# Kernel optimization log

Hardware: AMD Instinct MI355X
Metric: run time of the kernel (lower is better)

## Reference

```python
import jax, jax.numpy as jnp
import numpy as np

D_IN = 1024
D_OUT = 1024


def setup_inputs() -> dict:
    key = jax.random.key(0)
    ks = jax.random.split(key, 7)
    B, S = 4, 2048
    x = jax.random.normal(ks[0], (B, S, D_IN), dtype=jnp.float32)
    s = 1.0 / np.sqrt(D_IN)
    Wq = jax.random.uniform(ks[1], (D_IN, D_OUT), jnp.float32, -s, s)
    Wk = jax.random.uniform(ks[2], (D_IN, D_OUT), jnp.float32, -s, s)
    Wv = jax.random.uniform(ks[3], (D_IN, D_OUT), jnp.float32, -s, s)
    bq = jax.random.uniform(ks[4], (D_OUT,), jnp.float32, -s, s)
    bk = jax.random.uniform(ks[5], (D_OUT,), jnp.float32, -s, s)
    bv = jax.random.uniform(ks[6], (D_OUT,), jnp.float32, -s, s)
    return {"x": x, "Wq": Wq, "Wk": Wk, "Wv": Wv, "bq": bq, "bk": bk, "bv": bv}


def reference(x, Wq, Wk, Wv, bq, bk, bv):
    # x: [B, S, d_in]
    B, S, _ = x.shape
    q = x @ Wq + bq            # [B, S, d_out]
    k = x @ Wk + bk
    v = x @ Wv + bv
    scale = 1.0 / jnp.sqrt(jnp.asarray(q.shape[-1], q.dtype))
    scores = jnp.einsum('bqd,bkd->bqk', q, k)  # [B, S, S]
    causal = jnp.tril(jnp.ones((S, S), dtype=bool))
    scores = jnp.where(causal, scores, -jnp.inf)
    attn = jax.nn.softmax(scores * scale, axis=-1)
    return jnp.einsum('bqk,bkd->bqd', attn, v)
```

## Files before the change

### kernel.cpp

```cpp
#include <hip/hip_runtime.h>
#include <cstdint>

#define DEV __device__ __forceinline__

typedef __attribute__((ext_vector_type(4))) float f32x4;
typedef __attribute__((ext_vector_type(8))) short short8;
typedef __attribute__((ext_vector_type(4))) unsigned short u16x4;

constexpr int BS  = 4;
constexpr int SEQ = 2048;

DEV ushort f2b(float f){
  uint32_t u = __builtin_bit_cast(uint32_t, f);
  u += 0x7fffu + ((u >> 16) & 1u);
  return (ushort)(u >> 16);
}
DEV float b2f(ushort h){
  uint32_t u = (uint32_t)h << 16;
  return __builtin_bit_cast(float, u);
}

DEV void gload_lds16(const void* g, void* l){
  __builtin_amdgcn_global_load_lds(
      (const __attribute__((address_space(1))) unsigned int*)g,
      (__attribute__((address_space(3))) unsigned int*)l, 16, 0, 0);
}

#define BAR()    __builtin_amdgcn_s_barrier()
#define PRIO(x)  __builtin_amdgcn_s_setprio(x)
#define SCHEDB() __builtin_amdgcn_sched_barrier(0)
#define LGKM0()  asm volatile("s_waitcnt lgkmcnt(0)" ::: "memory")
#define WAITV(n) asm volatile("s_waitcnt vmcnt(" #n ")" ::: "memory")

__global__ __launch_bounds__(256) void convert_f2b8(const float* __restrict__ src,
                                                    ushort* __restrict__ dst){
  long i = (long)blockIdx.x * 256 + threadIdx.x;
  const f32x4* s4 = (const f32x4*)src;
  f32x4 a = s4[i*2], b = s4[i*2+1];
  short8 o;
  o[0]=(short)f2b(a[0]); o[1]=(short)f2b(a[1]); o[2]=(short)f2b(a[2]); o[3]=(short)f2b(a[3]);
  o[4]=(short)f2b(b[0]); o[5]=(short)f2b(b[1]); o[6]=(short)f2b(b[2]); o[7]=(short)f2b(b[3]);
  ((short8*)dst)[i] = o;
}

__global__ __launch_bounds__(256) void transpose_f2b(const float* __restrict__ src,
                                                     ushort* __restrict__ dst,
                                                     int R, int C){
  __shared__ float t[32][33];
  int c0 = blockIdx.x * 32, r0 = blockIdx.y * 32;
  int tx = threadIdx.x, ty = threadIdx.y;
  #pragma unroll
  for (int k=0;k<4;k++) t[ty+k*8][tx] = src[(long)(r0+ty+k*8)*C + c0+tx];
  __syncthreads();
  #pragma unroll
  for (int k=0;k<4;k++) dst[(long)(c0+ty+k*8)*R + r0+tx] = f2b(t[tx][ty+k*8]);
}

__global__ __launch_bounds__(256) void transpose_b2b(const ushort* __restrict__ src,
                                                     ushort* __restrict__ dst,
                                                     int R, int C){
  __shared__ ushort t[32][33];
  int c0 = blockIdx.x * 32, r0 = blockIdx.y * 32;
  int tx = threadIdx.x, ty = threadIdx.y;
  #pragma unroll
  for (int k=0;k<4;k++) t[ty+k*8][tx] = src[(long)(r0+ty+k*8)*C + c0+tx];
  __syncthreads();
  #pragma unroll
  for (int k=0;k<4;k++) dst[(long)(c0+ty+k*8)*R + r0+tx] = t[tx][ty+k*8];
}

struct GArgs {
  const ushort* A;  long lda; long aBS;
  const ushort* Bm; long ldb; long bBS;
  void* C;          long ldc; long cBS;
  const float* b0; const float* b1; const float* b2;
  int K;
};

__global__ __launch_bounds__(512, 2) void gemmA_qkv(GArgs g){
  extern __shared__ char sm[];
  const int tid = threadIdx.x;
  const int wid = tid >> 6, lane = tid & 63;
  const int wr = wid >> 2, wc = wid & 3;
  const int lr = lane & 15, lk = lane >> 4;
  const int f5 = ((lr >> 3) & 1) << 5;

  const int fid = blockIdx.x;
  const int xcd = fid & 7, j = fid >> 3;
  const int m0 = (xcd * 4 + (j & 3)) * 256;
  const int n0 = (j >> 2) * 192;

  const long lda2 = g.lda * 2, ldb2 = g.ldb * 2;
  const int skk = tid >> 8;
  const int srr = (tid >> 2) & 63;
  const int scc = tid & 3;
  const int scb = (scc * 16) ^ (((srr >> 3) & 1) << 5);
  const char* aU0 = (const char*)g.A  + (long)(m0       + srr)*lda2 + skk*64 + scb;
  const char* aU1 = (const char*)g.A  + (long)(m0 +  64 + srr)*lda2 + skk*64 + scb;
  const char* aU2 = (const char*)g.A  + (long)(m0 + 128 + srr)*lda2 + skk*64 + scb;
  const char* aU3 = (const char*)g.A  + (long)(m0 + 192 + srr)*lda2 + skk*64 + scb;
  const char* bU0 = (const char*)g.Bm + (long)(n0       + srr)*ldb2 + skk*64 + scb;
  const char* bU1 = (const char*)g.Bm + (long)(n0 +  64 + srr)*ldb2 + skk*64 + scb;
  const char* bU2 = (const char*)g.Bm + (long)(n0 + 128 + srr)*ldb2 + skk*64 + scb;
  const int dst = tid * 16;

#define STA(u, cb, k0) gload_lds16(aU##u + (k0)*2, sm + (cb)*57344 + u*8192 + dst)
#define STB(u, cb, k0) gload_lds16(bU##u + (k0)*2, sm + (cb)*57344 + 32768 + u*8192 + dst)

  int aoff[8], boff[3];
  #pragma unroll
  for (int mm=0;mm<8;mm++)
    aoff[mm] = wr*16384 + (mm>>2)*8192 + (mm&3)*1024 + lr*64 + ((lk*16) ^ f5);
  #pragma unroll
  for (int nn=0;nn<3;nn++){
    int br = wc*48 + nn*16 + lr;
    boff[nn] = 32768 + (br>>6)*8192 + (br&63)*64 + ((lk*16) ^ f5);
  }

  f32x4 acc[8][3];
  #pragma unroll
  for (int m=0;m<8;m++)
    #pragma unroll
    for (int n=0;n<3;n++) acc[m][n] = f32x4{0.f,0.f,0.f,0.f};

  const int NT = g.K >> 6;
  STA(0,0,0); STA(1,0,0); STA(2,0,0); STA(3,0,0);
  STB(0,0,0); STB(1,0,0); STB(2,0,0);
  STB(0,1,64); STB(1,1,64); STB(2,1,64);
  WAITV(3); BAR();

  short8 bf[3][2], af[2][2];
#define READ_AF(MB) \
    af[0][0] = *(const short8*)(base + aoff[MB  ]);        \
    af[0][1] = *(const short8*)(base + aoff[MB  ] + 4096); \
    af[1][0] = *(const short8*)(base + aoff[MB+1]);        \
    af[1][1] = *(const short8*)(base + aoff[MB+1] + 4096);
#define MFMA6(MB) \
    PRIO(1); \
    _Pragma("unroll") \
    for (int kk=0;kk<2;kk++) \
      _Pragma("unroll") \
      for (int mm=0;mm<2;mm++) \
        _Pragma("unroll") \
        for (int nn=0;nn<3;nn++) \
          acc[MB+mm][nn] = __builtin_amdgcn_mfma_f32_16x16x32_bf16(af[mm][kk], bf[nn][kk], acc[MB+mm][nn], 0,0,0); \
    PRIO(0);

  for (int t = 0; t < NT; ++t){
    const int c = t & 1;
    const char* base = sm + c*57344;
    const int kA = ((t+1) < NT ? (t+1) : NT-1) << 6;
    const int kB = ((t+2) < NT ? (t+2) : NT-1) << 6;
    STA(0, c^1, kA); STA(1, c^1, kA);
    #pragma unroll
    for (int nn=0;nn<3;nn++){
      bf[nn][0] = *(const short8*)(base + boff[nn]);
      bf[nn][1] = *(const short8*)(base + boff[nn] + 4096);
    }
    READ_AF(0);
    LGKM0(); SCHEDB();
    MFMA6(0);
    BAR();
    STA(2, c^1, kA); STA(3, c^1, kA);
    READ_AF(2);
    LGKM0(); SCHEDB();
    MFMA6(2);
    BAR();
    STB(0, c, kB); STB(1, c, kB);
    READ_AF(4);
    LGKM0(); SCHEDB();
    MFMA6(4);
    BAR();
    STB(2, c, kB);
    READ_AF(6);
    LGKM0(); SCHEDB();
    MFMA6(6);
    WAITV(3);
    BAR();
  }
  WAITV(0);
#undef STA
#undef STB
#undef READ_AF
#undef MFMA6

  #pragma unroll
  for (int nn=0;nn<3;nn++){
    int col  = n0 + wc*48 + nn*16 + lr;
    int sel  = col >> 10;
    int colq = col & 1023;
    const float* bp = (sel == 0) ? g.b0 : (sel == 1) ? g.b1 : g.b2;
    float bv = bp[colq];
    ushort* Cq = (ushort*)g.C + (long)sel * 8388608;
    #pragma unroll
    for (int mm=0;mm<8;mm++){
      int row0 = m0 + wr*128 + mm*16 + lk*4;
      #pragma unroll
      for (int i=0;i<4;i++)
        Cq[(long)(row0+i)*1024 + colq] = f2b(acc[mm][nn][i] + bv);
    }
  }
}

template<int MODE>
__global__ __launch_bounds__(512, 2) void gemmB(GArgs g){
  extern __shared__ char sm[];
  const int m0 = blockIdx.x * 128, n0 = blockIdx.y * 256;
  const int z  = blockIdx.z;
  if (MODE == 1 && n0 > m0 + 127) return;
  const int tid = threadIdx.x;
  const int wid = tid >> 6, lane = tid & 63;
  const int wr = wid >> 2, wc = wid & 3;
  const int lr = lane & 15, lk = lane >> 4;
  const int f5 = ((lr >> 3) & 1) << 5;

  const char* Ab = (const char*)(g.A  + (long)z * g.aBS);
  const char* Bb = (const char*)(g.Bm + (long)z * g.bBS);
  const long lda2 = g.lda * 2, ldb2 = g.ldb * 2;
  const int sr  = tid >> 2;
  const int scb = ((lane & 3) << 4) ^ (((sr >> 3) & 1) << 5);
  const char* ar0 = Ab + (long)(m0 + sr)*lda2 + scb;
  const char* br0 = Bb + (long)(n0 + sr      )*ldb2 + scb;
  const char* br1 = Bb + (long)(n0 + 128 + sr)*ldb2 + scb;
  const int dwo = wid << 10;

  auto ST = [&](const char* row, int c, int off, int k0){
    const char* p = row + k0*2;
    char* d = sm + c*49152 + off + dwo;
    gload_lds16(p,      d);
    gload_lds16(p + 64, d + 8192);
  };

  const int aoffs = (wr*64 + lr)*64 + ((lk*16) ^ f5);
  const int boffs = 16384 + (wc>>1)*16384 + ((wc&1)*64 + lr)*64 + ((lk*16) ^ f5);

  f32x4 acc[4][4];
  #pragma unroll
  for (int m=0;m<4;m++)
    #pragma unroll
    for (int n=0;n<4;n++) acc[m][n] = f32x4{0.f,0.f,0.f,0.f};

  const int Keff = (MODE == 2) ? (m0 + 128) : g.K;
  const int NT = Keff >> 6;
  ST(ar0, 0, 0, 0);
  ST(br0, 0, 16384, 0); ST(br1, 0, 32768, 0);
  ST(br0, 1, 16384, 64); ST(br1, 1, 32768, 64);
  WAITV(4); BAR();

  for (int t = 0; t < NT; ++t){
    const int c = t & 1;
    const char* base = sm + c*49152;
    const int kA = ((t+1) < NT ? (t+1) : NT-1) << 6;
    const int kB = ((t+2) < NT ? (t+2) : NT-1) << 6;
    short8 bf[4][2], af[2][2];
    ST(ar0, c^1, 0, kA);
    #pragma unroll
    for (int n=0;n<4;n++)
      #pragma unroll
      for (int kk=0;kk<2;kk++)
        bf[n][kk] = *(const short8*)(base + boffs + kk*8192 + n*1024);
    #pragma unroll
    for (int mm=0;mm<2;mm++)
      #pragma unroll
      for (int kk=0;kk<2;kk++)
        af[mm][kk] = *(const short8*)(base + aoffs + kk*8192 + mm*1024);
    LGKM0(); SCHEDB();
    PRIO(1);
    #pragma unroll
    for (int kk=0;kk<2;kk++)
      #pragma unroll
      for (int mm=0;mm<2;mm++)
        #pragma unroll
        for (int n=0;n<4;n++)
          acc[mm][n] = __builtin_amdgcn_mfma_f32_16x16x32_bf16(af[mm][kk], bf[n][kk], acc[mm][n], 0,0,0);
    PRIO(0);
    BAR();
    ST(br0, c, 16384, kB); ST(br1, c, 32768, kB);
    #pragma unroll
    for (int mm=0;mm<2;mm++)
      #pragma unroll
      for (int kk=0;kk<2;kk++)
        af[mm][kk] = *(const short8*)(base + aoffs + kk*8192 + (2+mm)*1024);
    LGKM0(); SCHEDB();
    PRIO(1);
    #pragma unroll
    for (int kk=0;kk<2;kk++)
      #pragma unroll
      for (int mm=0;mm<2;mm++)
        #pragma unroll
        for (int n=0;n<4;n++)
          acc[2+mm][n] = __builtin_amdgcn_mfma_f32_16x16x32_bf16(af[mm][kk], bf[n][kk], acc[2+mm][n], 0,0,0);
    PRIO(0);
    WAITV(4);
    BAR();
  }
  WAITV(0);

  long cz = (long)z * g.cBS;
  #pragma unroll
  for (int m=0;m<4;m++){
    int row0 = m0 + wr*64 + m*16 + lk*4;
    #pragma unroll
    for (int n=0;n<4;n++){
      int col = n0 + wc*64 + n*16 + lr;
      #pragma unroll
      for (int i=0;i<4;i++){
        long off = cz + (long)(row0+i)*g.ldc + col;
        if (MODE == 1) ((ushort*)g.C)[off] = f2b(acc[m][n][i]);
        else           ((float*)g.C)[off]  = acc[m][n][i];
      }
    }
  }
}

__global__ __launch_bounds__(256) void softmax_causal_b(const ushort* __restrict__ sc,
                                                        ushort* __restrict__ P){
  int row = blockIdx.x & (SEQ-1);
  int b   = blockIdx.x >> 11;
  const short8* srow = (const short8*)(sc + ((long)b*SEQ + row)*(long)SEQ);
  ushort* prow = P + ((long)b*SEQ + row)*(long)SEQ;
  int tid = threadIdx.x;
  int lane = tid & 63, wid = tid >> 6;
  const float scale = 0.03125f;
  float x[8]; float mx = -INFINITY;
  int base = tid * 8;
  if (base <= row){
    short8 v = srow[tid];
    #pragma unroll
    for (int j=0;j<8;j++){
      float t = (base + j <= row) ? b2f((ushort)v[j]) : -INFINITY;
      x[j] = t; mx = fmaxf(mx, t);
    }
  } else {
    #pragma unroll
    for (int j=0;j<8;j++) x[j] = -INFINITY;
  }
  #pragma unroll
  for (int off=1; off<64; off<<=1) mx = fmaxf(mx, __shfl_xor(mx, off));
  __shared__ float rb[8];
  if (lane == 0) rb[wid] = mx;
  __syncthreads();
  mx = fmaxf(fmaxf(rb[0],rb[1]), fmaxf(rb[2],rb[3]));
  float sum = 0.f; float e[8];
  #pragma unroll
  for (int i=0;i<8;i++){ e[i] = __expf((x[i]-mx)*scale); sum += e[i]; }
  #pragma unroll
  for (int off=1; off<64; off<<=1) sum += __shfl_xor(sum, off);
  if (lane == 0) rb[4+wid] = sum;
  __syncthreads();
  sum = (rb[4]+rb[5]) + (rb[6]+rb[7]);
  float inv = 1.0f / sum;
  int wlim = row | 127;
  if (base <= wlim){
    short8 o;
    #pragma unroll
    for (int j=0;j<8;j++) o[j] = (short)f2b(e[j]*inv);
    ((short8*)prow)[tid] = o;
  }
}

extern "C" void kernel_launch(void* const* d_in, const int* in_sizes, int n_in,
                              void* d_out, int out_size, void* d_ws, size_t ws_size,
                              hipStream_t stream){
  const float* x  = (const float*)d_in[0];
  const float* Wq = (const float*)d_in[1];
  const float* Wk = (const float*)d_in[2];
  const float* Wv = (const float*)d_in[3];
  const float* bq = (const float*)d_in[4];
  const float* bk = (const float*)d_in[5];
  const float* bv = (const float*)d_in[6];
  float* out = (float*)d_out;

  const long XB = 0;
  const long WT = 16777216;
  const long QB = 23068672;
  const long VT = 73400320;
  const long SC = 90177536;
  const long NEED = 157286400;
  const long PB = 0;
  if ((long)ws_size < NEED) return;

  char* ws = (char*)d_ws;
  ushort* xb = (ushort*)(ws + XB);
  ushort* wt = (ushort*)(ws + WT);
  ushort* qb = (ushort*)(ws + QB);
  ushort* kb = qb + 8388608;
  ushort* vb = qb + 16777216;
  ushort* vt = (ushort*)(ws + VT);
  ushort* sc = (ushort*)(ws + SC);
  ushort* pb = (ushort*)(ws + PB);

  hipFuncSetAttribute(reinterpret_cast<const void*>(&gemmA_qkv),
                      hipFuncAttributeMaxDynamicSharedMemorySize, 114688);
  hipFuncSetAttribute(reinterpret_cast<const void*>(&gemmB<1>),
                      hipFuncAttributeMaxDynamicSharedMemorySize, 98304);
  hipFuncSetAttribute(reinterpret_cast<const void*>(&gemmB<2>),
                      hipFuncAttributeMaxDynamicSharedMemorySize, 98304);

  dim3 tb(32, 8);

  convert_f2b8<<<4096, 256, 0, stream>>>(x, xb);
  transpose_f2b<<<dim3(32,32), tb, 0, stream>>>(Wq, wt + 0,       1024, 1024);
  transpose_f2b<<<dim3(32,32), tb, 0, stream>>>(Wk, wt + 1048576, 1024, 1024);
  transpose_f2b<<<dim3(32,32), tb, 0, stream>>>(Wv, wt + 2097152, 1024, 1024);

  GArgs pa{};
  pa.A = xb; pa.lda = 1024; pa.aBS = 0;
  pa.Bm = wt; pa.ldb = 1024; pa.bBS = 0;
  pa.C = (void*)qb; pa.ldc = 1024; pa.cBS = 0;
  pa.b0 = bq; pa.b1 = bk; pa.b2 = bv;
  pa.K = 1024;
  gemmA_qkv<<<512, 512, 114688, stream>>>(pa);

  transpose_b2b<<<dim3(32,256), tb, 0, stream>>>(vb, vt, 8192, 1024);

  GArgs sa{};
  sa.A = qb;  sa.lda = 1024; sa.aBS = (long)SEQ*1024;
  sa.Bm = kb; sa.ldb = 1024; sa.bBS = (long)SEQ*1024;
  sa.C = (void*)sc; sa.ldc = SEQ; sa.cBS = (long)SEQ*SEQ;
  sa.b0 = nullptr; sa.b1 = nullptr; sa.b2 = nullptr;
  sa.K = 1024;
  gemmB<1><<<dim3(16,8,4), 512, 98304, stream>>>(sa);

  softmax_causal_b<<<BS*SEQ, 256, 0, stream>>>(sc, pb);

  GArgs va{};
  va.A = pb;  va.lda = SEQ;  va.aBS = (long)SEQ*SEQ;
  va.Bm = vt; va.ldb = 8192; va.bBS = SEQ;
  va.C = (void*)out; va.ldc = 1024; va.cBS = (long)SEQ*1024;
  va.b0 = nullptr; va.b1 = nullptr; va.b2 = nullptr;
  va.K = SEQ;
  gemmB<2><<<dim3(16,4,4), 512, 98304, stream>>>(va);
}
```

Measured before the change: 173.8 us.

## Fuse exp into scores GEMM epilogue and defer softmax normalization to PV

```diff
diff --git a/kernel.cpp b/kernel.cpp
--- a/kernel.cpp
+++ b/kernel.cpp
@@ -30,6 +30,7 @@
 #define PRIO(x)  __builtin_amdgcn_s_setprio(x)
 #define SCHEDB() __builtin_amdgcn_sched_barrier(0)
 #define LGKM0()  asm volatile("s_waitcnt lgkmcnt(0)" ::: "memory")
+#define LGKM8()  asm volatile("s_waitcnt lgkmcnt(8)" ::: "memory")
 #define WAITV(n) asm volatile("s_waitcnt vmcnt(" #n ")" ::: "memory")
 
 __global__ __launch_bounds__(256) void convert_f2b8(const float* __restrict__ src,
@@ -43,17 +44,21 @@
   ((short8*)dst)[i] = o;
 }
 
-__global__ __launch_bounds__(256) void transpose_f2b(const float* __restrict__ src,
-                                                     ushort* __restrict__ dst,
-                                                     int R, int C){
+__global__ __launch_bounds__(256) void transpose_f2b3(const float* __restrict__ w0,
+                                                      const float* __restrict__ w1,
+                                                      const float* __restrict__ w2,
+                                                      ushort* __restrict__ dst){
   __shared__ float t[32][33];
+  const int zz = blockIdx.z;
+  const float* src = (zz == 0) ? w0 : (zz == 1) ? w1 : w2;
+  ushort* d = dst + (long)zz * 1048576;
   int c0 = blockIdx.x * 32, r0 = blockIdx.y * 32;
   int tx = threadIdx.x, ty = threadIdx.y;
   #pragma unroll
-  for (int k=0;k<4;k++) t[ty+k*8][tx] = src[(long)(r0+ty+k*8)*C + c0+tx];
+  for (int k=0;k<4;k++) t[ty+k*8][tx] = src[(long)(r0+ty+k*8)*1024 + c0+tx];
   __syncthreads();
   #pragma unroll
-  for (int k=0;k<4;k++) dst[(long)(c0+ty+k*8)*R + r0+tx] = f2b(t[tx][ty+k*8]);
+  for (int k=0;k<4;k++) d[(long)(c0+ty+k*8)*1024 + r0+tx] = f2b(t[tx][ty+k*8]);
 }
 
 __global__ __launch_bounds__(256) void transpose_b2b(const ushort* __restrict__ src,
@@ -202,12 +207,154 @@
   }
 }
 
-template<int MODE>
-__global__ __launch_bounds__(512, 2) void gemmB(GArgs g){
+__global__ __launch_bounds__(512, 2) void scores8p(GArgs g){
+  extern __shared__ char sm[];
+  const int m0 = blockIdx.x * 256, n0 = blockIdx.y * 256;
+  const int z  = blockIdx.z;
+  if (n0 > m0) return;
+  const int tid = threadIdx.x;
+  const int wid = tid >> 6, lane = tid & 63;
+  const int wr = wid >> 2, wc = wid & 3;
+  const int lr = lane & 15, lk = lane >> 4;
+
+  const char* Ab = (const char*)(g.A  + (long)z * g.aBS);
+  const char* Bb = (const char*)(g.Bm + (long)z * g.bBS);
+  const long lda2 = g.lda * 2, ldb2 = g.ldb * 2;
+  const int srow = tid >> 2;
+  const int scol = ((tid & 3) << 4) ^ (((tid >> 5) & 1) << 5);
+  const char* sA = Ab + (long)(m0 + srow) * lda2 + scol;
+  const char* sB = Bb + (long)(n0 + srow) * ldb2 + scol;
+  const int dst16 = tid << 4;
+
+  auto STAGE = [&](int tt, int which){
+    const char* s = (which < 2)
+        ? sA + (long)(which & 1) * 128 * lda2 + (long)tt * 128
+        : sB + (long)(which & 1) * 128 * ldb2 + (long)tt * 128;
+    char* d = sm + (tt & 1) * 65536 + which * 16384 + dst16;
+    gload_lds16(s,      d);
+    gload_lds16(s + 64, d + 8192);
+  };
+
+  int aoff[8], boff[4];
+  #pragma unroll
+  for (int mm = 0; mm < 8; mm++){
+    int r = mm * 16 + lr;
+    aoff[mm] = wr * 16384 + r * 64 + ((lk * 16) ^ (((r >> 3) & 1) << 5));
+  }
+  #pragma unroll
+  for (int nn = 0; nn < 4; nn++){
+    int rb = wc * 64 + nn * 16 + lr;
+    boff[nn] = 32768 + (rb >> 7) * 16384 + (rb & 127) * 64
+             + ((lk * 16) ^ (((rb >> 3) & 1) << 5));
+  }
+
+  f32x4 acc[8][4];
+  #pragma unroll
+  for (int m = 0; m < 8; m++)
+    #pragma unroll
+    for (int n = 0; n < 4; n++) acc[m][n] = f32x4{0.f,0.f,0.f,0.f};
+
+  const int NT = g.K >> 6;
+  STAGE(0,2); STAGE(0,3); STAGE(0,0); STAGE(0,1);
+  STAGE(1,2); STAGE(1,3);
+  WAITV(4); BAR();
+
+  short8 af[2][2], bf[4][2];
+#define READ_A(MB) \
+    af[0][0] = *(const short8*)(base + aoff[MB]);            \
+    af[0][1] = *(const short8*)(base + aoff[MB] + 8192);     \
+    af[1][0] = *(const short8*)(base + aoff[MB+1]);          \
+    af[1][1] = *(const short8*)(base + aoff[MB+1] + 8192);
+#define MFMA16(MB) \
+    PRIO(1); \
+    _Pragma("unroll") \
+    for (int kk = 0; kk < 2; kk++) \
+      _Pragma("unroll") \
+      for (int mm = 0; mm < 2; mm++) \
+        _Pragma("unroll") \
+        for (int nn = 0; nn < 4; nn++) \
+          acc[MB+mm][nn] = __builtin_amdgcn_mfma_f32_16x16x32_bf16(af[mm][kk], bf[nn][kk], acc[MB+mm][nn], 0,0,0); \
+    PRIO(0);
+
+  for (int t = 0; t < NT; ++t){
+    const char* base = sm + (t & 1) * 65536;
+    if (t + 1 < NT) STAGE(t+1, 0);
+    #pragma unroll
+    for (int nn = 0; nn < 4; nn++){
+      bf[nn][0] = *(const short8*)(base + boff[nn]);
+      bf[nn][1] = *(const short8*)(base + boff[nn] + 8192);
+    }
+    READ_A(0);
+    LGKM8();
+    SCHEDB(); BAR(); LGKM0(); SCHEDB();
+    MFMA16(0);
+    SCHEDB(); BAR();
+    if (t + 1 < NT) STAGE(t+1, 1);
+    READ_A(2);
+    SCHEDB(); BAR(); LGKM0(); SCHEDB();
+    MFMA16(2);
+    SCHEDB(); BAR();
+    if (t + 2 < NT) STAGE(t+2, 2);
+    READ_A(4);
+    SCHEDB(); BAR(); LGKM0(); SCHEDB();
+    MFMA16(4);
+    SCHEDB(); BAR();
+    if (t + 2 < NT) STAGE(t+2, 3);
+    READ_A(6);
+    SCHEDB(); BAR(); LGKM0(); SCHEDB();
+    MFMA16(6);
+    WAITV(4);
+    SCHEDB(); BAR();
+  }
+#undef READ_A
+#undef MFMA16
+
+  const float scale = 0.03125f;
+  ushort* Cs = (ushort*)g.C + (long)z * g.cBS;
+  #pragma unroll
+  for (int mm = 0; mm < 8; mm++){
+    int row0 = m0 + wr*128 + mm*16 + lk*4;
+    #pragma unroll
+    for (int nn = 0; nn < 4; nn++){
+      int col = n0 + wc*64 + nn*16 + lr;
+      #pragma unroll
+      for (int i = 0; i < 4; i++){
+        int row = row0 + i;
+        float e = (col <= row) ? __expf(acc[mm][nn][i] * scale) : 0.0f;
+        Cs[(long)row*g.ldc + col] = f2b(e);
+      }
+    }
+  }
+}
+
+__global__ __launch_bounds__(256) void rowsum_inv(const ushort* __restrict__ P,
+                                                  float* __restrict__ inv){
+  int row = blockIdx.x & (SEQ-1);
+  int b   = blockIdx.x >> 11;
+  const short8* pr = (const short8*)(P + ((long)b*SEQ + row)*(long)SEQ);
+  int tid = threadIdx.x;
+  int lane = tid & 63, wid = tid >> 6;
+  float s = 0.f;
+  if (tid*8 <= row){
+    short8 v = pr[tid];
+    #pragma unroll
+    for (int j=0;j<8;j++) s += b2f((ushort)v[j]);
+  }
+  #pragma unroll
+  for (int off=1; off<64; off<<=1) s += __shfl_xor(s, off);
+  __shared__ float rb[4];
+  if (lane == 0) rb[wid] = s;
+  __syncthreads();
+  if (tid == 0){
+    float tot = (rb[0]+rb[1]) + (rb[2]+rb[3]);
+    inv[(long)b*SEQ + row] = 1.0f / tot;
+  }
+}
+
+__global__ __launch_bounds__(512, 2) void gemmPV(GArgs g){
   extern __shared__ char sm[];
   const int m0 = blockIdx.x * 128, n0 = blockIdx.y * 256;
   const int z  = blockIdx.z;
-  if (MODE == 1 && n0 > m0 + 127) return;
   const int tid = threadIdx.x;
   const int wid = tid >> 6, lane = tid & 63;
   const int wr = wid >> 2, wc = wid & 3;
@@ -240,7 +387,7 @@
     #pragma unroll
     for (int n=0;n<4;n++) acc[m][n] = f32x4{0.f,0.f,0.f,0.f};
 
-  const int Keff = (MODE == 2) ? (m0 + 128) : g.K;
+  const int Keff = m0 + 128;
   const int NT = Keff >> 6;
   ST(ar0, 0, 0, 0);
   ST(br0, 0, 16384, 0); ST(br1, 0, 32768, 0);
@@ -296,6 +443,7 @@
   }
   WAITV(0);
 
+  const float* invp = g.b0 + (long)z * SEQ;
   long cz = (long)z * g.cBS;
   #pragma unroll
   for (int m=0;m<4;m++){
@@ -304,58 +452,9 @@
     for (int n=0;n<4;n++){
       int col = n0 + wc*64 + n*16 + lr;
       #pragma unroll
-      for (int i=0;i<4;i++){
-        long off = cz + (long)(row0+i)*g.ldc + col;
-        if (MODE == 1) ((ushort*)g.C)[off] = f2b(acc[m][n][i]);
-        else           ((float*)g.C)[off]  = acc[m][n][i];
-      }
+      for (int i=0;i<4;i++)
+        ((float*)g.C)[cz + (long)(row0+i)*g.ldc + col] = acc[m][n][i] * invp[row0+i];
     }
-  }
-}
-
-__global__ __launch_bounds__(256) void softmax_causal_b(const ushort* __restrict__ sc,
-                                                        ushort* __restrict__ P){
-  int row = blockIdx.x & (SEQ-1);
-  int b   = blockIdx.x >> 11;
-  const short8* srow = (const short8*)(sc + ((long)b*SEQ + row)*(long)SEQ);
-  ushort* prow = P + ((long)b*SEQ + row)*(long)SEQ;
-  int tid = threadIdx.x;
-  int lane = tid & 63, wid = tid >> 6;
-  const float scale = 0.03125f;
-  float x[8]; float mx = -INFINITY;
-  int base = tid * 8;
-  if (base <= row){
-    short8 v = srow[tid];
-    #pragma unroll
-    for (int j=0;j<8;j++){
-      float t = (base + j <= row) ? b2f((ushort)v[j]) : -INFINITY;
-      x[j] = t; mx = fmaxf(mx, t);
-    }
-  } else {
-    #pragma unroll
-    for (int j=0;j<8;j++) x[j] = -INFINITY;
-  }
-  #pragma unroll
-  for (int off=1; off<64; off<<=1) mx = fmaxf(mx, __shfl_xor(mx, off));
-  __shared__ float rb[8];
-  if (lane == 0) rb[wid] = mx;
-  __syncthreads();
-  mx = fmaxf(fmaxf(rb[0],rb[1]), fmaxf(rb[2],rb[3]));
-  float sum = 0.f; float e[8];
-  #pragma unroll
-  for (int i=0;i<8;i++){ e[i] = __expf((x[i]-mx)*scale); sum += e[i]; }
-  #pragma unroll
-  for (int off=1; off<64; off<<=1) sum += __shfl_xor(sum, off);
-  if (lane == 0) rb[4+wid] = sum;
-  __syncthreads();
-  sum = (rb[4]+rb[5]) + (rb[6]+rb[7]);
-  float inv = 1.0f / sum;
-  int wlim = row | 127;
-  if (base <= wlim){
-    short8 o;
-    #pragma unroll
-    for (int j=0;j<8;j++) o[j] = (short)f2b(e[j]*inv);
-    ((short8*)prow)[tid] = o;
   }
 }
 
@@ -375,9 +474,9 @@
   const long WT = 16777216;
   const long QB = 23068672;
   const long VT = 73400320;
-  const long SC = 90177536;
-  const long NEED = 157286400;
-  const long PB = 0;
+  const long PU = 90177536;
+  const long IV = 123731968;
+  const long NEED = 123764736;
   if ((long)ws_size < NEED) return;
 
   char* ws = (char*)d_ws;
@@ -387,22 +486,20 @@
   ushort* kb = qb + 8388608;
   ushort* vb = qb + 16777216;
   ushort* vt = (ushort*)(ws + VT);
-  ushort* sc = (ushort*)(ws + SC);
-  ushort* pb = (ushort*)(ws + PB);
+  ushort* pu = (ushort*)(ws + PU);
+  float*  iv = (float* )(ws + IV);
 
   hipFuncSetAttribute(reinterpret_cast<const void*>(&gemmA_qkv),
                       hipFuncAttributeMaxDynamicSharedMemorySize, 114688);
-  hipFuncSetAttribute(reinterpret_cast<const void*>(&gemmB<1>),
+  hipFuncSetAttribute(reinterpret_cast<const void*>(&scores8p),
+                      hipFuncAttributeMaxDynamicSharedMemorySize, 131072);
+  hipFuncSetAttribute(reinterpret_cast<const void*>(&gemmPV),
                       hipFuncAttributeMaxDynamicSharedMemorySize, 98304);
-  hipFuncSetAttribute(reinterpret_cast<const void*>(&gemmB<2>),
-                      hipFuncAttributeMaxDynamicSharedMemorySize, 98304);
 
   dim3 tb(32, 8);
 
   convert_f2b8<<<4096, 256, 0, stream>>>(x, xb);
-  transpose_f2b<<<dim3(32,32), tb, 0, stream>>>(Wq, wt + 0,       1024, 1024);
-  transpose_f2b<<<dim3(32,32), tb, 0, stream>>>(Wk, wt + 1048576, 1024, 1024);
-  transpose_f2b<<<dim3(32,32), tb, 0, stream>>>(Wv, wt + 2097152, 1024, 1024);
+  transpose_f2b3<<<dim3(32,32,3), tb, 0, stream>>>(Wq, Wk, Wv, wt);
 
   GArgs pa{};
   pa.A = xb; pa.lda = 1024; pa.aBS = 0;
@@ -417,18 +514,18 @@
   GArgs sa{};
   sa.A = qb;  sa.lda = 1024; sa.aBS = (long)SEQ*1024;
   sa.Bm = kb; sa.ldb = 1024; sa.bBS = (long)SEQ*1024;
-  sa.C = (void*)sc; sa.ldc = SEQ; sa.cBS = (long)SEQ*SEQ;
+  sa.C = (void*)pu; sa.ldc = SEQ; sa.cBS = (long)SEQ*SEQ;
   sa.b0 = nullptr; sa.b1 = nullptr; sa.b2 = nullptr;
   sa.K = 1024;
-  gemmB<1><<<dim3(16,8,4), 512, 98304, stream>>>(sa);
-
-  softmax_causal_b<<<BS*SEQ, 256, 0, stream>>>(sc, pb);
+  scores8p<<<dim3(8,8,4), 512, 131072, stream>>>(sa);
+
+  rowsum_inv<<<BS*SEQ, 256, 0, stream>>>(pu, iv);
 
   GArgs va{};
-  va.A = pb;  va.lda = SEQ;  va.aBS = (long)SEQ*SEQ;
+  va.A = pu;  va.lda = SEQ;  va.aBS = (long)SEQ*SEQ;
   va.Bm = vt; va.ldb = 8192; va.bBS = SEQ;
   va.C = (void*)out; va.ldc = 1024; va.cBS = (long)SEQ*1024;
-  va.b0 = nullptr; va.b1 = nullptr; va.b2 = nullptr;
+  va.b0 = iv; va.b1 = nullptr; va.b2 = nullptr;
   va.K = SEQ;
-  gemmB<2><<<dim3(16,4,4), 512, 98304, stream>>>(va);
-}
+  gemmPV<<<dim3(16,4,4), 512, 98304, stream>>>(va);
+}
```

Result: faster. 169.5 us (-2.5%).
